# Performance work log

Hardware: AMD Instinct MI355X
Metric: run time of the kernel (lower is better)

The kernel has to match this reference:

```python
import jax, jax.numpy as jnp
import numpy as np

BN_EPS = 1e-5


def setup_inputs() -> dict:
    key = jax.random.key(0)
    ks = jax.random.split(key, 12)
    B, N, d_e, d_a = 16, 2048, 256, 64
    s_e = 1.0 / np.sqrt(d_e)
    return {
        "x":    jax.random.normal(ks[0], (B, N, d_e), dtype=jnp.float32),
        "Wq":   jax.random.uniform(ks[1], (d_e, d_a), jnp.float32, -s_e, s_e),
        "bq":   jax.random.uniform(ks[2], (d_a,), jnp.float32, -s_e, s_e),
        "Wk":   jax.random.uniform(ks[3], (d_e, d_a), jnp.float32, -s_e, s_e),
        "bk":   jax.random.uniform(ks[4], (d_a,), jnp.float32, -s_e, s_e),
        "Wv":   jax.random.uniform(ks[5], (d_e, d_e), jnp.float32, -s_e, s_e),
        "bv":   jax.random.uniform(ks[6], (d_e,), jnp.float32, -s_e, s_e),
        "Wl":   jax.random.uniform(ks[7], (d_e, d_e), jnp.float32, -s_e, s_e),
        "bl":   jax.random.uniform(ks[8], (d_e,), jnp.float32, -s_e, s_e),
        "gamma": jnp.ones((d_e,), jnp.float32),
        "beta":  jnp.zeros((d_e,), jnp.float32),
    }


def reference(x, Wq, bq, Wk, bk, Wv, bv, Wl, bl, gamma, beta):
    # x: [B, N, d_e]
    q = x @ Wq + bq          # [B, N, d_a]
    k = x @ Wk + bk          # [B, N, d_a]
    v = x @ Wv + bv          # [B, N, d_e]
    d_a = q.shape[-1]
    # NOTE: PCT scales by d_a, not sqrt(d_a) -- faithful to the source.
    score = jnp.einsum('bnd,bmd->bnm', q, k) / jnp.asarray(d_a, q.dtype)
    score = jax.nn.softmax(score, axis=2)          # [B, N, N]
    attn = jnp.einsum('bnm,bmd->bnd', score, v)    # [B, N, d_e]
    # LBR: linear + BatchNorm1d (training-mode batch stats over B,N) + ReLU
    h = attn @ Wl + bl                             # [B, N, d_e]
    mean = jnp.mean(h, axis=(0, 1))
    var = jnp.mean((h - mean) ** 2, axis=(0, 1))   # biased variance (torch BN)
    y = jax.nn.relu((h - mean) * jax.lax.rsqrt(var + BN_EPS) * gamma + beta)
    return y + x
```

## Files before the change

kernel.cpp:

```cpp
#include <hip/hip_runtime.h>
#include <hip/hip_bf16.h>

#define B_  16
#define N_  2048
#define DE  256
#define DA  64
#define T_  (B_*N_)

typedef __attribute__((ext_vector_type(4)))  float f32x4;
typedef __attribute__((ext_vector_type(8)))  short bf16x8;
typedef unsigned short u16;

__device__ __forceinline__ float bf2f(u16 x){
  unsigned v = ((unsigned)x) << 16;
  return __builtin_bit_cast(float, v);
}
__device__ __forceinline__ u16 f2bf(float f){
  unsigned u = __builtin_bit_cast(unsigned, f);
  u += 0x7fffu + ((u >> 16) & 1u);
  return (u16)(u >> 16);
}
__device__ __forceinline__ f32x4 mfma16(bf16x8 a, bf16x8 b, f32x4 c){
  return __builtin_amdgcn_mfma_f32_16x16x32_bf16(a, b, c, 0, 0, 0);
}
__device__ __forceinline__ bool is_f32(const void* gsig){
  return *(const unsigned*)gsig == 0x3F800000u;
}
__device__ __forceinline__ float gload(const void* p, long i, bool f32m){
  return f32m ? ((const float*)p)[i] : bf2f(((const u16*)p)[i]);
}

__global__ void k_prep(const void* __restrict__ Wq, const void* __restrict__ Wk,
                       const void* __restrict__ Wv, const void* __restrict__ Wl,
                       const void* __restrict__ bq, const void* __restrict__ bk,
                       const void* __restrict__ bv, const void* __restrict__ bl,
                       const void* __restrict__ gsig,
                       u16* __restrict__ Wt, u16* __restrict__ Wlt,
                       float* __restrict__ bqkv, float* __restrict__ blf){
  bool f32m = is_f32(gsig);
  int i = blockIdx.x*256 + threadIdx.x;
  if (i < 384*256){
    int n = i/256, kk = i%256;
    float v;
    if (n < 64)       v = gload(Wq, (long)kk*64 + n, f32m);
    else if (n < 128) v = gload(Wk, (long)kk*64 + (n-64), f32m);
    else              v = gload(Wv, (long)kk*256 + (n-128), f32m);
    Wt[i] = f2bf(v);
  }
  int j = i - 384*256;
  if (j >= 0 && j < 256*256){
    int n = j/256, kk = j%256;
    Wlt[j] = f2bf(gload(Wl, (long)kk*256 + n, f32m));
  }
  int m = i - (384*256 + 256*256);
  if (m >= 0 && m < 384){
    float v;
    if (m < 64)       v = gload(bq, m, f32m);
    else if (m < 128) v = gload(bk, m-64, f32m);
    else              v = gload(bv, m-128, f32m);
    bqkv[m] = v;
  }
  int p = i - (384*256 + 256*256 + 384);
  if (p >= 0 && p < 256) blf[p] = gload(bl, p, f32m);
}

__global__ __launch_bounds__(256) void k_qkv(
    const void* __restrict__ xg, const void* __restrict__ gsig,
    const u16* __restrict__ Wt, const float* __restrict__ bqkv,
    u16* __restrict__ qo, u16* __restrict__ ko, u16* __restrict__ vtt){
  __shared__ __align__(16) u16 sm[256*72];
  bool f32m = is_f32(gsig);
  int tid = threadIdx.x, lane = tid & 63, w = tid >> 6;
  int lm = lane & 15, lq = lane >> 4;
  long t0 = (long)blockIdx.x * 64;

  #pragma unroll
  for(int it=0; it<8; it++){
    int c = tid + 256*it;
    int tok = c >> 5, kk = (c & 31)*8;
    bf16x8 d;
    if (f32m){
      const float* xf = (const float*)xg + (t0+tok)*DE + kk;
      f32x4 a = *(const f32x4*)xf;
      f32x4 b2 = *(const f32x4*)(xf+4);
      #pragma unroll
      for(int j2=0;j2<4;j2++){ d[j2]=(short)f2bf(a[j2]); d[4+j2]=(short)f2bf(b2[j2]); }
    } else {
      d = *(const bf16x8*)((const u16*)xg + (t0+tok)*DE + kk);
    }
    *(bf16x8*)(sm + tok*264 + kk) = d;
  }
  __syncthreads();

  f32x4 acc[4][6];
  #pragma unroll
  for(int mt=0;mt<4;mt++)
    #pragma unroll
    for(int nt=0;nt<6;nt++){ acc[mt][nt][0]=0.f;acc[mt][nt][1]=0.f;acc[mt][nt][2]=0.f;acc[mt][nt][3]=0.f; }

  for(int s=0;s<8;s++){
    int kk = s*32 + lq*8;
    bf16x8 afr[4];
    #pragma unroll
    for(int mt=0;mt<4;mt++)
      afr[mt] = *(const bf16x8*)(sm + (mt*16+lm)*264 + kk);
    #pragma unroll
    for(int nt=0;nt<6;nt++){
      int col = w*96 + nt*16 + lm;
      bf16x8 bfr = *(const bf16x8*)(Wt + (long)col*DE + kk);
      #pragma unroll
      for(int mt=0;mt<4;mt++)
        acc[mt][nt] = mfma16(afr[mt], bfr, acc[mt][nt]);
    }
  }
  __syncthreads();

  #pragma unroll
  for(int nt=0;nt<6;nt++){
    int col = w*96 + nt*16 + lm;
    float bias = bqkv[col];
    #pragma unroll
    for(int mt=0;mt<4;mt++){
      #pragma unroll
      for(int r=0;r<4;r++){
        int tokin = mt*16 + lq*4 + r;
        u16 o = f2bf(acc[mt][nt][r] + bias);
        if (col < 64)        qo[(t0+tokin)*DA + col]      = o;
        else if (col < 128)  ko[(t0+tokin)*DA + (col-64)] = o;
        else                 sm[(col-128)*72 + tokin]     = o;
      }
    }
  }
  __syncthreads();
  int b = (int)(t0 >> 11), kt = (int)((t0 & 2047) >> 6);
  u16* tile = vtt + (long)(b*32 + kt)*16384;
  #pragma unroll
  for(int g=0; g<8; g++){
    bf16x8 d = *(const bf16x8*)(sm + tid*72 + g*8);
    *(bf16x8*)(tile + tid*64 + g*8) = d;
  }
}

__global__ __launch_bounds__(256, 2) void k_attn(
    const u16* __restrict__ qg, const u16* __restrict__ kg,
    const u16* __restrict__ vtt, u16* __restrict__ attng){
  __shared__ __align__(16) u16 P[2][64*72];
  __shared__ float lred[4][64];

  int bid = blockIdx.x;
  int b  = 2*(bid & 7) + ((bid >> 3) >> 5);
  int qb = (bid >> 3) & 31;
  int tid = threadIdx.x, lane = tid & 63, w = tid >> 6;
  int lm = lane & 15, lq = lane >> 4;

  long kb0 = (long)b * N_;
  long rb  = kb0 + qb*64;

  const u16* qbase = qg + rb*DA;
  bf16x8 qf[4][2];
  #pragma unroll
  for(int rt=0;rt<4;rt++)
    #pragma unroll
    for(int s=0;s<2;s++)
      qf[rt][s] = *(const bf16x8*)(qbase + (long)(rt*16+lm)*DA + s*32 + lq*8);

  f32x4 o[4][4];
  #pragma unroll
  for(int rt=0;rt<4;rt++)
    #pragma unroll
    for(int nt=0;nt<4;nt++){ o[rt][nt][0]=0.f;o[rt][nt][1]=0.f;o[rt][nt][2]=0.f;o[rt][nt][3]=0.f; }
  float ls[4][4];
  #pragma unroll
  for(int rt=0;rt<4;rt++)
    #pragma unroll
    for(int r=0;r<4;r++) ls[rt][r] = 0.f;

  const u16* kptr = kg  + (kb0 + 16*w + lm)*DA + lq*8;
  const u16* vptr = vtt + (long)b*524288 + (64*w + lm)*64 + lq*8;

  auto phaseA = [&](int t, int pb){
    const u16* kr = kptr + (long)t*64*DA;
    bf16x8 kf0 = *(const bf16x8*)(kr);
    bf16x8 kf1 = *(const bf16x8*)(kr + 32);
    #pragma unroll
    for(int rt=0;rt<4;rt++){
      f32x4 S; S[0]=0.f;S[1]=0.f;S[2]=0.f;S[3]=0.f;
      S = mfma16(qf[rt][0], kf0, S);
      S = mfma16(qf[rt][1], kf1, S);
      #pragma unroll
      for(int r=0;r<4;r++){
        float e = __expf(S[r] * 0.015625f);
        ls[rt][r] += e;
        P[pb][(rt*16 + lq*4 + r)*72 + 16*w + lm] = f2bf(e);
      }
    }
  };

  phaseA(0, 0);
  for(int t=0; t<N_/64; t++){
    __syncthreads();
    if (t < N_/64 - 1) phaseA(t+1, (t+1)&1);
    int pb = t & 1;
    const u16* vt_t = vptr + (long)t*16384;
    bf16x8 pf[4][2];
    #pragma unroll
    for(int rt=0;rt<4;rt++)
      #pragma unroll
      for(int s=0;s<2;s++)
        pf[rt][s] = *(const bf16x8*)(&P[pb][(rt*16+lm)*72 + s*32 + lq*8]);
    #pragma unroll
    for(int nt=0;nt<4;nt++){
      bf16x8 vf0 = *(const bf16x8*)(vt_t + nt*1024);
      bf16x8 vf1 = *(const bf16x8*)(vt_t + nt*1024 + 32);
      #pragma unroll
      for(int rt=0;rt<4;rt++){
        o[rt][nt] = mfma16(pf[rt][0], vf0, o[rt][nt]);
        o[rt][nt] = mfma16(pf[rt][1], vf1, o[rt][nt]);
      }
    }
  }

  #pragma unroll
  for(int rt=0;rt<4;rt++)
    #pragma unroll
    for(int r=0;r<4;r++){
      float s = ls[rt][r];
      s += __shfl_xor(s, 1, 64);
      s += __shfl_xor(s, 2, 64);
      s += __shfl_xor(s, 4, 64);
      s += __shfl_xor(s, 8, 64);
      ls[rt][r] = s;
    }
  if (lm == 0){
    #pragma unroll
    for(int rt=0;rt<4;rt++)
      #pragma unroll
      for(int r=0;r<4;r++)
        lred[w][rt*16 + lq*4 + r] = ls[rt][r];
  }
  __syncthreads();
  u16* abase = attng + rb*DE + 64*w;
  #pragma unroll
  for(int rt=0;rt<4;rt++){
    #pragma unroll
    for(int r=0;r<4;r++){
      int row = rt*16 + lq*4 + r;
      float inv = 1.0f / (lred[0][row] + lred[1][row] + lred[2][row] + lred[3][row]);
      #pragma unroll
      for(int nt=0;nt<4;nt++)
        abase[(long)row*DE + nt*16 + lm] = f2bf(o[rt][nt][r] * inv);
    }
  }
}

__global__ __launch_bounds__(256) void k_hgemm(
    const u16* __restrict__ attng, const u16* __restrict__ Wlt,
    const float* __restrict__ blf, u16* __restrict__ hg, float* __restrict__ stats){
  __shared__ __align__(16) u16 xs[64*264];
  int tid = threadIdx.x, lane = tid & 63, w = tid >> 6;
  int lm = lane & 15, lq = lane >> 4;
  long t0 = (long)blockIdx.x * 64;

  const u16* src = attng + t0*DE;
  #pragma unroll
  for(int i=0;i<8;i++){
    int c16 = tid + 256*i;
    int tok = c16 >> 5, kk = (c16 & 31)*8;
    *(bf16x8*)(xs + tok*264 + kk) = *(const bf16x8*)(src + (long)tok*DE + kk);
  }
  __syncthreads();

  f32x4 acc[4][4];
  #pragma unroll
  for(int mt=0;mt<4;mt++)
    #pragma unroll
    for(int nt=0;nt<4;nt++){ acc[mt][nt][0]=0.f;acc[mt][nt][1]=0.f;acc[mt][nt][2]=0.f;acc[mt][nt][3]=0.f; }

  for(int s=0;s<8;s++){
    int kk = s*32 + lq*8;
    bf16x8 afr[4];
    #pragma unroll
    for(int mt=0;mt<4;mt++)
      afr[mt] = *(const bf16x8*)(xs + (mt*16+lm)*264 + kk);
    #pragma unroll
    for(int nt=0;nt<4;nt++){
      int col = w*64 + nt*16 + lm;
      bf16x8 bfr = *(const bf16x8*)(Wlt + (long)col*DE + kk);
      #pragma unroll
      for(int mt=0;mt<4;mt++)
        acc[mt][nt] = mfma16(afr[mt], bfr, acc[mt][nt]);
    }
  }
  #pragma unroll
  for(int nt=0;nt<4;nt++){
    int col = w*64 + nt*16 + lm;
    float bias = blf[col];
    float s1 = 0.f, s2 = 0.f;
    #pragma unroll
    for(int mt=0;mt<4;mt++){
      #pragma unroll
      for(int r=0;r<4;r++){
        long tok = t0 + mt*16 + lq*4 + r;
        float val = acc[mt][nt][r] + bias;
        hg[tok*DE + col] = f2bf(val);
        s1 += val; s2 += val*val;
      }
    }
    s1 += __shfl_xor(s1, 16, 64); s2 += __shfl_xor(s2, 16, 64);
    s1 += __shfl_xor(s1, 32, 64); s2 += __shfl_xor(s2, 32, 64);
    if (lq == 0){
      atomicAdd(&stats[col], s1);
      atomicAdd(&stats[256 + col], s2);
    }
  }
}

__global__ void k_params(const float* __restrict__ stats, const void* __restrict__ gamma,
                         const void* __restrict__ beta, float* __restrict__ params){
  bool f32m = is_f32(gamma);
  int ch = threadIdx.x;
  const float inv_n = 1.0f/32768.0f;
  float mean = stats[ch]*inv_n;
  float var  = stats[256+ch]*inv_n - mean*mean;
  float sc = gload(gamma, ch, f32m) * rsqrtf(var + 1e-5f);
  params[ch] = sc;
  params[256+ch] = gload(beta, ch, f32m) - mean*sc;
}

__global__ __launch_bounds__(256) void k_apply(
    const u16* __restrict__ hg, const void* __restrict__ xg,
    const void* __restrict__ gsig,
    const float* __restrict__ params, void* __restrict__ outg){
  bool f32m = is_f32(gsig);
  long i = (long)blockIdx.x*256 + threadIdx.x;
  long base = i*8;
  int ch0 = (int)(base & 255);
  bf16x8 hv = *(const bf16x8*)(hg + base);
  f32x4 sc0 = *(const f32x4*)(params + ch0);
  f32x4 sc1 = *(const f32x4*)(params + ch0 + 4);
  f32x4 sh0 = *(const f32x4*)(params + 256 + ch0);
  f32x4 sh1 = *(const f32x4*)(params + 256 + ch0 + 4);
  float xv[8];
  if (f32m){
    f32x4 a = *((const f32x4*)xg + i*2);
    f32x4 b2 = *((const f32x4*)xg + i*2 + 1);
    #pragma unroll
    for(int j=0;j<4;j++){ xv[j]=a[j]; xv[4+j]=b2[j]; }
  } else {
    bf16x8 xb = *((const bf16x8*)xg + i);
    #pragma unroll
    for(int j=0;j<8;j++) xv[j] = bf2f((u16)xb[j]);
  }
  float y[8];
  #pragma unroll
  for(int j=0;j<8;j++){
    float h = bf2f((u16)hv[j]);
    float sc = (j<4) ? sc0[j] : sc1[j-4];
    float sh = (j<4) ? sh0[j] : sh1[j-4];
    y[j] = fmaxf(h*sc + sh, 0.f) + xv[j];
  }
  if (f32m){
    f32x4 o0, o1;
    #pragma unroll
    for(int j=0;j<4;j++){ o0[j]=y[j]; o1[j]=y[4+j]; }
    *((f32x4*)outg + i*2) = o0;
    *((f32x4*)outg + i*2 + 1) = o1;
  } else {
    bf16x8 ov;
    #pragma unroll
    for(int j=0;j<8;j++) ov[j] = (short)f2bf(y[j]);
    *((bf16x8*)outg + i) = ov;
  }
}

extern "C" void kernel_launch(void* const* d_in, const int* in_sizes, int n_in,
                              void* d_out, int out_size, void* d_ws, size_t ws_size,
                              hipStream_t stream){
  const void* x     = d_in[0];
  const void* Wq    = d_in[1];
  const void* bq    = d_in[2];
  const void* Wk    = d_in[3];
  const void* bk    = d_in[4];
  const void* Wv    = d_in[5];
  const void* bv    = d_in[6];
  const void* Wl    = d_in[7];
  const void* bl    = d_in[8];
  const void* gamma = d_in[9];
  const void* beta  = d_in[10];

  char* ws = (char*)d_ws;
  u16*   Wt    = (u16*)  (ws + 0x0);
  u16*   Wlt   = (u16*)  (ws + 0x30000);
  float* bqkv  = (float*)(ws + 0x50000);
  float* blf   = (float*)(ws + 0x50600);
  float* stats = (float*)(ws + 0x50A00);
  float* params= (float*)(ws + 0x51200);
  u16*   qw    = (u16*)  (ws + 0x60000);
  u16*   kw    = (u16*)  (ws + 0x460000);
  u16*   vtt   = (u16*)  (ws + 0x860000);
  u16*   attnw = (u16*)  (ws + 0x1860000);
  u16*   hw    = (u16*)  (ws + 0x2860000);

  hipMemsetAsync(stats, 0, 512*sizeof(float), stream);
  k_prep  <<<643, 256, 0, stream>>>(Wq, Wk, Wv, Wl, bq, bk, bv, bl, gamma, Wt, Wlt, bqkv, blf);
  k_qkv   <<<512, 256, 0, stream>>>(x, gamma, Wt, bqkv, qw, kw, vtt);
  k_attn  <<<512, 256, 0, stream>>>(qw, kw, vtt, attnw);
  k_hgemm <<<512, 256, 0, stream>>>(attnw, Wlt, blf, hw, stats);
  k_params<<<1, 256, 0, stream>>>(stats, gamma, beta, params);
  k_apply <<<4096, 256, 0, stream>>>(hw, x, gamma, params, d_out);
}
```

Measured before the change: 250.2 us.

## Register double-buffer K/V tiles and restructure attention loop barrier

The attention loop now prefetches the next iteration's K and V fragments into a two-slot register buffer while the current QK^T, exp and PV MMAs run. It also drops the one-step software pipelining of the score phase. Scores for the current tile go to LDS and are read back after a raw s_waitcnt+s_barrier. This aims to hide global load latency for K/V behind compute, at the cost of more VGPRs and less overlap between the exp/LDS phase and the PV MMAs. A single barrier per iteration with double-buffered P still has to protect against write-after-read across iterations.

```diff
diff --git a/kernel.cpp b/kernel.cpp
--- a/kernel.cpp
+++ b/kernel.cpp
@@ -178,46 +178,60 @@
   const u16* kptr = kg  + (kb0 + 16*w + lm)*DA + lq*8;
   const u16* vptr = vtt + (long)b*524288 + (64*w + lm)*64 + lq*8;
 
-  auto phaseA = [&](int t, int pb){
-    const u16* kr = kptr + (long)t*64*DA;
-    bf16x8 kf0 = *(const bf16x8*)(kr);
-    bf16x8 kf1 = *(const bf16x8*)(kr + 32);
+  bf16x8 kr[2][2];
+  bf16x8 vr[2][4][2];
+  kr[0][0] = *(const bf16x8*)(kptr);
+  kr[0][1] = *(const bf16x8*)(kptr + 32);
+  #pragma unroll
+  for(int nt=0;nt<4;nt++){
+    vr[0][nt][0] = *(const bf16x8*)(vptr + nt*1024);
+    vr[0][nt][1] = *(const bf16x8*)(vptr + nt*1024 + 32);
+  }
+
+  for(int t=0; t<N_/64; t++){
+    int cb = t & 1, nb = cb ^ 1;
+    f32x4 S[4];
     #pragma unroll
     for(int rt=0;rt<4;rt++){
-      f32x4 S; S[0]=0.f;S[1]=0.f;S[2]=0.f;S[3]=0.f;
-      S = mfma16(qf[rt][0], kf0, S);
-      S = mfma16(qf[rt][1], kf1, S);
+      f32x4 a4; a4[0]=0.f;a4[1]=0.f;a4[2]=0.f;a4[3]=0.f;
+      a4 = mfma16(qf[rt][0], kr[cb][0], a4);
+      a4 = mfma16(qf[rt][1], kr[cb][1], a4);
+      S[rt] = a4;
+    }
+    if (t < N_/64 - 1){
+      const u16* kn = kptr + (long)(t+1)*64*DA;
+      kr[nb][0] = *(const bf16x8*)(kn);
+      kr[nb][1] = *(const bf16x8*)(kn + 32);
+      const u16* vn = vptr + (long)(t+1)*16384;
+      #pragma unroll
+      for(int nt=0;nt<4;nt++){
+        vr[nb][nt][0] = *(const bf16x8*)(vn + nt*1024);
+        vr[nb][nt][1] = *(const bf16x8*)(vn + nt*1024 + 32);
+      }
+    }
+    #pragma unroll
+    for(int rt=0;rt<4;rt++){
       #pragma unroll
       for(int r=0;r<4;r++){
-        float e = __expf(S[r] * 0.015625f);
+        float e = __expf(S[rt][r] * 0.015625f);
         ls[rt][r] += e;
-        P[pb][(rt*16 + lq*4 + r)*72 + 16*w + lm] = f2bf(e);
+        P[cb][(rt*16 + lq*4 + r)*72 + 16*w + lm] = f2bf(e);
       }
     }
-  };
-
-  phaseA(0, 0);
-  for(int t=0; t<N_/64; t++){
-    __syncthreads();
-    if (t < N_/64 - 1) phaseA(t+1, (t+1)&1);
-    int pb = t & 1;
-    const u16* vt_t = vptr + (long)t*16384;
+    asm volatile("s_waitcnt lgkmcnt(0)\n\ts_barrier" ::: "memory");
     bf16x8 pf[4][2];
     #pragma unroll
     for(int rt=0;rt<4;rt++)
       #pragma unroll
       for(int s=0;s<2;s++)
-        pf[rt][s] = *(const bf16x8*)(&P[pb][(rt*16+lm)*72 + s*32 + lq*8]);
-    #pragma unroll
-    for(int nt=0;nt<4;nt++){
-      bf16x8 vf0 = *(const bf16x8*)(vt_t + nt*1024);
-      bf16x8 vf1 = *(const bf16x8*)(vt_t + nt*1024 + 32);
+        pf[rt][s] = *(const bf16x8*)(&P[cb][(rt*16+lm)*72 + s*32 + lq*8]);
+    #pragma unroll
+    for(int nt=0;nt<4;nt++)
       #pragma unroll
       for(int rt=0;rt<4;rt++){
-        o[rt][nt] = mfma16(pf[rt][0], vf0, o[rt][nt]);
-        o[rt][nt] = mfma16(pf[rt][1], vf1, o[rt][nt]);
+        o[rt][nt] = mfma16(pf[rt][0], vr[cb][nt][0], o[rt][nt]);
+        o[rt][nt] = mfma16(pf[rt][1], vr[cb][nt][1], o[rt][nt]);
       }
-    }
   }
 
   #pragma unroll
```

After: 659.3 us. 164% more time.

## Double-buffer K/V tiles in registers and use lighter LDS-only barrier

Applied to the files above, without the earlier changes.

Restructures the attention main loop to prefetch the next tile's K and V fragments into a second register set while the current tile is computed. The loop is unrolled by two with ping-pong buffers for both registers and P in LDS. The __syncthreads is replaced with an inline-asm barrier that waits only on LDS counters, so outstanding global loads can stay in flight across it. This aims to hide global-load latency of K/V behind MFMA and exp work. The cost is more VGPRs for the two V buffers, which may reduce occupancy, and the score step no longer overlaps with the previous tile's P·V across the barrier.

```diff
diff --git a/kernel.cpp b/kernel.cpp
--- a/kernel.cpp
+++ b/kernel.cpp
@@ -178,47 +178,60 @@
   const u16* kptr = kg  + (kb0 + 16*w + lm)*DA + lq*8;
   const u16* vptr = vtt + (long)b*524288 + (64*w + lm)*64 + lq*8;
 
-  auto phaseA = [&](int t, int pb){
-    const u16* kr = kptr + (long)t*64*DA;
-    bf16x8 kf0 = *(const bf16x8*)(kr);
-    bf16x8 kf1 = *(const bf16x8*)(kr + 32);
-    #pragma unroll
-    for(int rt=0;rt<4;rt++){
-      f32x4 S; S[0]=0.f;S[1]=0.f;S[2]=0.f;S[3]=0.f;
-      S = mfma16(qf[rt][0], kf0, S);
-      S = mfma16(qf[rt][1], kf1, S);
-      #pragma unroll
-      for(int r=0;r<4;r++){
-        float e = __expf(S[r] * 0.015625f);
-        ls[rt][r] += e;
-        P[pb][(rt*16 + lq*4 + r)*72 + 16*w + lm] = f2bf(e);
-      }
-    }
-  };
-
-  phaseA(0, 0);
-  for(int t=0; t<N_/64; t++){
-    __syncthreads();
-    if (t < N_/64 - 1) phaseA(t+1, (t+1)&1);
-    int pb = t & 1;
-    const u16* vt_t = vptr + (long)t*16384;
-    bf16x8 pf[4][2];
-    #pragma unroll
-    for(int rt=0;rt<4;rt++)
-      #pragma unroll
-      for(int s=0;s<2;s++)
-        pf[rt][s] = *(const bf16x8*)(&P[pb][(rt*16+lm)*72 + s*32 + lq*8]);
-    #pragma unroll
-    for(int nt=0;nt<4;nt++){
-      bf16x8 vf0 = *(const bf16x8*)(vt_t + nt*1024);
-      bf16x8 vf1 = *(const bf16x8*)(vt_t + nt*1024 + 32);
-      #pragma unroll
-      for(int rt=0;rt<4;rt++){
-        o[rt][nt] = mfma16(pf[rt][0], vf0, o[rt][nt]);
-        o[rt][nt] = mfma16(pf[rt][1], vf1, o[rt][nt]);
-      }
-    }
-  }
+  bf16x8 kA0,kA1, kB0,kB1;
+  bf16x8 vA[4][2], vB[4][2];
+
+  #define PREF(t_, K0_, K1_, V_) {                              \
+    const u16* kn_ = kptr + (long)(t_)*64*DA;                   \
+    K0_ = *(const bf16x8*)(kn_);                                \
+    K1_ = *(const bf16x8*)(kn_ + 32);                           \
+    const u16* vn_ = vptr + (long)(t_)*16384;                   \
+    _Pragma("unroll")                                           \
+    for(int nt=0;nt<4;nt++){                                    \
+      V_[nt][0] = *(const bf16x8*)(vn_ + nt*1024);              \
+      V_[nt][1] = *(const bf16x8*)(vn_ + nt*1024 + 32);         \
+    } }
+
+  #define PHASE_A(K0_, K1_, pb_) {                              \
+    _Pragma("unroll")                                           \
+    for(int rt=0;rt<4;rt++){                                    \
+      f32x4 a4; a4[0]=0.f;a4[1]=0.f;a4[2]=0.f;a4[3]=0.f;        \
+      a4 = mfma16(qf[rt][0], K0_, a4);                          \
+      a4 = mfma16(qf[rt][1], K1_, a4);                          \
+      _Pragma("unroll")                                         \
+      for(int r=0;r<4;r++){                                     \
+        float e_ = __expf(a4[r] * 0.015625f);                   \
+        ls[rt][r] += e_;                                        \
+        P[pb_][(rt*16 + lq*4 + r)*72 + 16*w + lm] = f2bf(e_);   \
+      } } }
+
+  #define PHASE_B(V_, pb_) {                                    \
+    _Pragma("unroll")                                           \
+    for(int rt=0;rt<4;rt++){                                    \
+      bf16x8 pf0 = *(const bf16x8*)(&P[pb_][(rt*16+lm)*72 + lq*8]);      \
+      bf16x8 pf1 = *(const bf16x8*)(&P[pb_][(rt*16+lm)*72 + 32 + lq*8]); \
+      _Pragma("unroll")                                         \
+      for(int nt=0;nt<4;nt++){                                  \
+        o[rt][nt] = mfma16(pf0, V_[nt][0], o[rt][nt]);          \
+        o[rt][nt] = mfma16(pf1, V_[nt][1], o[rt][nt]);          \
+      } } }
+
+  #define LDS_BARRIER asm volatile("s_waitcnt lgkmcnt(0)\n\ts_barrier" ::: "memory")
+
+  PREF(0, kA0, kA1, vA);
+  for(int t=0; t<N_/64; t+=2){
+    PREF(t+1, kB0, kB1, vB);
+    PHASE_A(kA0, kA1, 0);
+    LDS_BARRIER;
+    PHASE_B(vA, 0);
+    if (t+2 < N_/64) PREF(t+2, kA0, kA1, vA);
+    PHASE_A(kB0, kB1, 1);
+    LDS_BARRIER;
+    PHASE_B(vB, 1);
+  }
+  #undef PREF
+  #undef PHASE_A
+  #undef PHASE_B
 
   #pragma unroll
   for(int rt=0;rt<4;rt++)
```

Result: no change. 250.4 us (+0.1%).
